# Kernel tuning notes

Measured on AMD Instinct MI355X. Metric: run time of the kernel, lower is better.

## Reference

```python
import jax, jax.numpy as jnp
import numpy as np

N, DEG, F_IN, F_OUT, H = 8192, 16, 1024, 128, 8


def setup_inputs() -> dict:
    key = jax.random.key(0)
    ks = jax.random.split(key, 6)
    features = jax.random.normal(ks[0], (N, F_IN), dtype=jnp.float32)
    adj = jax.random.randint(ks[1], (N, DEG), 0, N)  # fixed-degree adjacency
    W = jax.random.normal(ks[2], (H, F_IN, F_OUT), dtype=jnp.float32) / np.sqrt(F_IN)
    bW = jax.random.normal(ks[3], (H, F_OUT), dtype=jnp.float32) * 0.01
    a = jax.random.normal(ks[4], (H, 2 * F_OUT), dtype=jnp.float32) / np.sqrt(2.0 * F_OUT)
    ba = jax.random.normal(ks[5], (H,), dtype=jnp.float32) * 0.01
    return {"features": features, "adj": adj, "W": W, "bW": bW, "a": a, "ba": ba}


def reference(features, adj, W, bW, a, ba):
    n = features.shape[0]
    # neighbors with self appended last (matches adjlist[node] + [node])
    nbr = jnp.concatenate([adj, jnp.arange(n)[:, None]], axis=1)  # [N, DEG+1]
    # per-head linear transform: h[k] = features @ W_k + b_k
    h = jnp.einsum('nf,hfo->hno', features, W) + bW[:, None, :]  # [H, N, F_OUT]
    # attention score a_k([h_dst, h_src]) + bias decomposed into dst/src parts
    a_dst, a_src = a[:, :F_OUT], a[:, F_OUT:]
    s_dst = jnp.einsum('hno,ho->hn', h, a_dst)  # [H, N]
    s_src = jnp.einsum('hno,ho->hn', h, a_src)  # [H, N]
    scores = s_dst[:, :, None] + s_src[:, nbr] + ba[:, None, None]  # [H, N, DEG+1]
    scores = jax.nn.leaky_relu(scores, 0.2)
    alpha = jax.nn.softmax(scores, axis=-1)  # softmax over neighbors (incl. self)
    h_src = h[:, nbr]  # [H, N, DEG+1, F_OUT]
    out = jnp.einsum('hnd,hndf->hnf', alpha, h_src)  # [H, N, F_OUT]
    # concat heads along feature dim -> [N, H*F_OUT]
    return out.transpose(1, 0, 2).reshape(n, H * F_OUT)
```

## Files before the change

### kernel.cpp

```cpp
#include <hip/hip_runtime.h>
#include <hip/hip_bf16.h>

#define N_NODES 8192
#define DEG     16
#define F_IN    1024
#define F_OUT   128
#define NH      8

typedef __bf16 bf16x8 __attribute__((ext_vector_type(8)));
typedef float  f32x4  __attribute__((ext_vector_type(4)));

__device__ __forceinline__ float bf2f(unsigned short u) {
    union { unsigned int i; float f; } v;
    v.i = ((unsigned int)u) << 16;
    return v.f;
}
__device__ __forceinline__ unsigned short f2bf(float f) {
    union { float f; unsigned int u; } v; v.f = f;
    unsigned int u = v.u + 0x7FFFu + ((v.u >> 16) & 1u);
    return (unsigned short)(u >> 16);
}
__device__ __forceinline__ int detect_bf16(const unsigned int* __restrict__ w) {
    int hits = 0;
#pragma unroll
    for (int i = 0; i < 64; ++i) {
        unsigned int x = w[i * 131 + 17];
        int e = (x >> 7) & 0xFF;
        hits += (e >= 100 && e <= 140) ? 1 : 0;
    }
    return hits > 32;
}
__device__ __forceinline__ float rd_scalar(const void* p, int idx, int isbf) {
    return isbf ? bf2f(((const unsigned short*)p)[idx]) : ((const float*)p)[idx];
}
__device__ __forceinline__ void gload16(const void* g, void* l) {
    __builtin_amdgcn_global_load_lds(
        (const __attribute__((address_space(1))) void*)g,
        (__attribute__((address_space(3))) void*)l, 16, 0, 0);
}

__global__ __launch_bounds__(256) void prep_inputs(
    const void* __restrict__ feat, const void* __restrict__ W,
    unsigned short* __restrict__ featb, unsigned short* __restrict__ Wt)
{
    const int isbf = detect_bf16((const unsigned int*)feat);
    if (blockIdx.x < 4096) {
        size_t i8 = ((size_t)blockIdx.x * 256 + threadIdx.x) * 8;
        if (isbf) {
            *(uint4*)(featb + i8) = ((const uint4*)feat)[i8 / 8];
        } else {
            const float* s = (const float*)feat + i8;
            float4 u0 = *(const float4*)s;
            float4 u1 = *(const float4*)(s + 4);
            unsigned short t[8] = { f2bf(u0.x), f2bf(u0.y), f2bf(u0.z), f2bf(u0.w),
                                    f2bf(u1.x), f2bf(u1.y), f2bf(u1.z), f2bf(u1.w) };
            *(uint4*)(featb + i8) = *(const uint4*)t;
        }
    } else {
        __shared__ float tile[64][65];
        const int bx = blockIdx.x - 4096;
        const int h  = bx >> 5;
        const int kt = (bx >> 1) & 15;
        const int ot = bx & 1;
        const int t  = threadIdx.x;
#pragma unroll
        for (int i = 0; i < 16; ++i) {
            int id = i * 256 + t, r = id >> 6, c = id & 63;
            tile[r][c] = rd_scalar(W, ((h * 1024 + kt * 64 + r) * 128) + ot * 64 + c, isbf);
        }
        __syncthreads();
#pragma unroll
        for (int i = 0; i < 16; ++i) {
            int id = i * 256 + t, oc = id >> 6, kc = id & 63;
            Wt[(size_t)(h * 128 + ot * 64 + oc) * 1024 + kt * 64 + kc] = f2bf(tile[kc][oc]);
        }
    }
}

__global__ __launch_bounds__(512, 4) void gat_gemm6(
    const unsigned short* __restrict__ featb,
    const unsigned short* __restrict__ Wt,
    const void* __restrict__ raw_feat,
    const void* __restrict__ bW, const void* __restrict__ a,
    const void* __restrict__ ba,
    __hip_bfloat16* __restrict__ hbuf,
    float* __restrict__ sdst, float* __restrict__ ssrc)
{
    const int rawbf = detect_bf16((const unsigned int*)raw_feat);

    const int h   = blockIdx.y;
    const int bxp = ((blockIdx.x & 7) << 3) | (blockIdx.x >> 3);
    const int n0  = bxp * 128;
    const int tid = threadIdx.x;

    __shared__ __align__(16) unsigned short As[2][128 * 64];
    __shared__ __align__(16) unsigned short Bs[2][128 * 64];

    const int lane = tid & 63;
    const int wave = tid >> 6;
    const int wr   = wave >> 1;
    const int wc   = wave & 1;
    const int quad = lane >> 4;
    const int l16  = lane & 15;
    const int sw   = l16 & 7;
    const int srow   = lane >> 3;
    const int schunk = lane & 7;

    f32x4 acc[2][4];
#pragma unroll
    for (int i = 0; i < 2; ++i)
#pragma unroll
        for (int j = 0; j < 4; ++j) acc[i][j] = (f32x4)0.f;

    const unsigned short* wbase = Wt + (size_t)h * F_OUT * F_IN;

    for (int k0 = 0; k0 < F_IN; k0 += 128) {
#pragma unroll
        for (int p = 0; p < 2; ++p) {
            const int kk0 = k0 + p * 64;
#pragma unroll
            for (int t = 0; t < 2; ++t) {
                const int r0  = t * 64 + wave * 8;
                const int row = r0 + srow;
                const int gc  = schunk ^ (row & 7);
                gload16(&featb[(size_t)(n0 + row) * F_IN + kk0 + gc * 8],
                        &As[p][r0 * 64]);
                gload16(&wbase[(size_t)row * F_IN + kk0 + gc * 8],
                        &Bs[p][r0 * 64]);
            }
        }
        __syncthreads();

#pragma unroll
        for (int p = 0; p < 2; ++p) {
#pragma unroll
            for (int ks = 0; ks < 2; ++ks) {
                const int kc = ks * 4 + quad;
                const int cs = (kc ^ sw) * 8;
                bf16x8 af[2], bfr[4];
#pragma unroll
                for (int rt = 0; rt < 2; ++rt)
                    af[rt] = *(const bf16x8*)&As[p][(wr * 32 + rt * 16 + l16) * 64 + cs];
#pragma unroll
                for (int ct = 0; ct < 4; ++ct)
                    bfr[ct] = *(const bf16x8*)&Bs[p][(wc * 64 + ct * 16 + l16) * 64 + cs];
#pragma unroll
                for (int rt = 0; rt < 2; ++rt)
#pragma unroll
                    for (int ct = 0; ct < 4; ++ct)
                        acc[rt][ct] = __builtin_amdgcn_mfma_f32_16x16x32_bf16(
                            af[rt], bfr[ct], acc[rt][ct], 0, 0, 0);
            }
        }
        __syncthreads();
    }

#pragma unroll
    for (int ct = 0; ct < 4; ++ct) {
        const int col = wc * 64 + ct * 16 + l16;
        const float bwv = rd_scalar(bW, h * F_OUT + col, rawbf);
#pragma unroll
        for (int rt = 0; rt < 2; ++rt) {
            const int nrow = n0 + wr * 32 + rt * 16 + quad * 4;
            __hip_bfloat16* dst = hbuf + ((size_t)h * N_NODES + nrow) * F_OUT + col;
#pragma unroll
            for (int r = 0; r < 4; ++r)
                dst[(size_t)r * F_OUT] = __float2bfloat16(acc[rt][ct][r] + bwv);
        }
    }

    float adst[4], asrc[4];
#pragma unroll
    for (int ct = 0; ct < 4; ++ct) {
        const int col = wc * 64 + ct * 16 + l16;
        adst[ct] = rd_scalar(a, h * 256 + col, rawbf);
        asrc[ct] = rd_scalar(a, h * 256 + 128 + col, rawbf);
    }
    float pd[2][4] = {}, ps[2][4] = {};
#pragma unroll
    for (int rt = 0; rt < 2; ++rt)
#pragma unroll
        for (int ct = 0; ct < 4; ++ct)
#pragma unroll
            for (int r = 0; r < 4; ++r) {
                pd[rt][r] += acc[rt][ct][r] * adst[ct];
                ps[rt][r] += acc[rt][ct][r] * asrc[ct];
            }
#pragma unroll
    for (int off = 1; off < 16; off <<= 1)
#pragma unroll
        for (int rt = 0; rt < 2; ++rt)
#pragma unroll
            for (int r = 0; r < 4; ++r) {
                pd[rt][r] += __shfl_xor(pd[rt][r], off, 64);
                ps[rt][r] += __shfl_xor(ps[rt][r], off, 64);
            }

    float* sred = (float*)&As[0][0];
    if (l16 == 0) {
#pragma unroll
        for (int rt = 0; rt < 2; ++rt)
#pragma unroll
            for (int r = 0; r < 4; ++r) {
                const int row32 = rt * 16 + quad * 4 + r;
                sred[((wr * 2 + wc) * 2 + 0) * 32 + row32] = pd[rt][r];
                sred[((wr * 2 + wc) * 2 + 1) * 32 + row32] = ps[rt][r];
            }
    }
    __syncthreads();
    if (wc == 0 && lane < 32) {
        const float bav = rd_scalar(ba, h, rawbf);
        const float vd = sred[((wr * 2 + 0) * 2 + 0) * 32 + lane]
                       + sred[((wr * 2 + 1) * 2 + 0) * 32 + lane] + bav;
        const float vs = sred[((wr * 2 + 0) * 2 + 1) * 32 + lane]
                       + sred[((wr * 2 + 1) * 2 + 1) * 32 + lane];
        const int nrow = n0 + wr * 32 + lane;
        sdst[h * N_NODES + nrow] = vd;
        ssrc[h * N_NODES + nrow] = vs;
    }
}

__global__ __launch_bounds__(256) void gat_aggr4(
    const unsigned short* __restrict__ hbuf,
    const int* __restrict__ adj,
    const float* __restrict__ sdst, const float* __restrict__ ssrc,
    const void* __restrict__ raw_feat, void* __restrict__ out)
{
    const int isbf = detect_bf16((const unsigned int*)raw_feat);
    const int h    = blockIdx.x;
    const int wave = threadIdx.x >> 6;
    const int lane = threadIdx.x & 63;
    const int half = lane >> 5;
    const int l32  = lane & 31;
    const int n    = blockIdx.y * 8 + wave * 2 + half;

    int nbr = n;
    if (l32 < DEG) nbr = adj[n * DEG + l32];

    float s = -1e30f;
    if (l32 < 17) {
        float sv = sdst[h * N_NODES + n] + ssrc[h * N_NODES + nbr];
        s = sv > 0.f ? sv : 0.2f * sv;
    }
    float m = s;
#pragma unroll
    for (int off = 1; off < 32; off <<= 1)
        m = fmaxf(m, __shfl_xor(m, off, 64));
    float ev = (l32 < 17) ? __expf(s - m) : 0.f;
    float sum = ev;
#pragma unroll
    for (int off = 1; off < 32; off <<= 1)
        sum += __shfl_xor(sum, off, 64);
    ev *= (1.f / sum);

    const unsigned short* hb = hbuf + (size_t)h * N_NODES * F_OUT;
    const int fc    = l32 * 4;
    const int sbase = half << 5;
    float a0 = 0.f, a1 = 0.f, a2 = 0.f, a3 = 0.f;
#pragma unroll
    for (int d = 0; d < 17; ++d) {
        const int   nb = __shfl(nbr, sbase + d, 64);
        const float av = __shfl(ev,  sbase + d, 64);
        uint2 pk = *(const uint2*)&hb[(size_t)nb * F_OUT + fc];
        a0 += av * bf2f((unsigned short)(pk.x & 0xffffu));
        a1 += av * bf2f((unsigned short)(pk.x >> 16));
        a2 += av * bf2f((unsigned short)(pk.y & 0xffffu));
        a3 += av * bf2f((unsigned short)(pk.y >> 16));
    }

    const size_t oidx = (size_t)n * (NH * F_OUT) + h * F_OUT + fc;
    if (isbf) {
        uint2 res;
        res.x = (unsigned int)f2bf(a0) | ((unsigned int)f2bf(a1) << 16);
        res.y = (unsigned int)f2bf(a2) | ((unsigned int)f2bf(a3) << 16);
        *(uint2*)&((unsigned short*)out)[oidx] = res;
    } else {
        float4 res = { a0, a1, a2, a3 };
        *(float4*)&((float*)out)[oidx] = res;
    }
}

__global__ __launch_bounds__(256) void gat_gemm_fb(
    const void* __restrict__ feat, const void* __restrict__ W,
    const void* __restrict__ bW, __hip_bfloat16* __restrict__ hbuf)
{
    const int isbf = detect_bf16((const unsigned int*)feat);
    const int h = blockIdx.y, n0 = blockIdx.x * 128, tid = threadIdx.x;
    __shared__ __align__(16) unsigned short As[128][72];
    __shared__ __align__(16) unsigned short Bs[128][72];
    const int lane = tid & 63, wave = tid >> 6, quad = lane >> 4, l16 = lane & 15;
    f32x4 acc[2][8];
#pragma unroll
    for (int i = 0; i < 2; ++i)
#pragma unroll
        for (int j = 0; j < 8; ++j) acc[i][j] = (f32x4)0.f;
    for (int k0 = 0; k0 < F_IN; k0 += 64) {
        if (isbf) {
            const unsigned short* fbase = (const unsigned short*)feat + (size_t)n0 * F_IN;
            const unsigned short* wsrc  = (const unsigned short*)W +
                                          (size_t)h * F_IN * F_OUT + (size_t)k0 * F_OUT;
#pragma unroll
            for (int t = 0; t < 4; ++t) {
                int c = t * 256 + tid, row = c >> 3, kc = c & 7;
                *(uint4*)&As[row][kc * 8] = *(const uint4*)&fbase[row * F_IN + k0 + kc * 8];
            }
#pragma unroll
            for (int t = 0; t < 2; ++t) {
                int c = t * 256 + tid, kr2 = c >> 4, mm = c & 15, oc = mm * 8;
                uint4 w0 = *(const uint4*)&wsrc[(2 * kr2) * F_OUT + oc];
                uint4 w1 = *(const uint4*)&wsrc[(2 * kr2 + 1) * F_OUT + oc];
                const unsigned short* p0 = (const unsigned short*)&w0;
                const unsigned short* p1 = (const unsigned short*)&w1;
#pragma unroll
                for (int j = 0; j < 8; ++j) {
                    int i = (j + mm) & 7;
                    *(unsigned int*)&Bs[oc + i][2 * kr2] =
                        (unsigned int)p0[i] | ((unsigned int)p1[i] << 16);
                }
            }
        } else {
            const float* fbase = (const float*)feat + (size_t)n0 * F_IN;
            const float* wsrc  = (const float*)W +
                                 (size_t)h * F_IN * F_OUT + (size_t)k0 * F_OUT;
#pragma unroll
            for (int t = 0; t < 4; ++t) {
                int c = t * 256 + tid, row = c >> 3, kc = c & 7;
                const float* src = &fbase[row * F_IN + k0 + kc * 8];
                float4 u0 = *(const float4*)src, u1 = *(const float4*)(src + 4);
                unsigned short sh[8] = { f2bf(u0.x), f2bf(u0.y), f2bf(u0.z), f2bf(u0.w),
                                         f2bf(u1.x), f2bf(u1.y), f2bf(u1.z), f2bf(u1.w) };
                *(uint4*)&As[row][kc * 8] = *(const uint4*)sh;
            }
#pragma unroll
            for (int t = 0; t < 2; ++t) {
                int c = t * 256 + tid, kr2 = c >> 4, mm = c & 15, oc = mm * 8;
                const float* r0 = &wsrc[(2 * kr2) * F_OUT + oc];
                const float* r1 = &wsrc[(2 * kr2 + 1) * F_OUT + oc];
                float4 e0 = *(const float4*)r0, e1 = *(const float4*)(r0 + 4);
                float4 o0 = *(const float4*)r1, o1 = *(const float4*)(r1 + 4);
                unsigned short p0[8] = { f2bf(e0.x), f2bf(e0.y), f2bf(e0.z), f2bf(e0.w),
                                         f2bf(e1.x), f2bf(e1.y), f2bf(e1.z), f2bf(e1.w) };
                unsigned short p1[8] = { f2bf(o0.x), f2bf(o0.y), f2bf(o0.z), f2bf(o0.w),
                                         f2bf(o1.x), f2bf(o1.y), f2bf(o1.z), f2bf(o1.w) };
#pragma unroll
                for (int j = 0; j < 8; ++j) {
                    int i = (j + mm) & 7;
                    *(unsigned int*)&Bs[oc + i][2 * kr2] =
                        (unsigned int)p0[i] | ((unsigned int)p1[i] << 16);
                }
            }
        }
        __syncthreads();
#pragma unroll
        for (int ks = 0; ks < 2; ++ks) {
            const int kk = ks * 32 + quad * 8;
            bf16x8 af[2], bfr[8];
#pragma unroll
            for (int rt = 0; rt < 2; ++rt)
                af[rt] = *(const bf16x8*)&As[wave * 32 + rt * 16 + l16][kk];
#pragma unroll
            for (int ct = 0; ct < 8; ++ct)
                bfr[ct] = *(const bf16x8*)&Bs[ct * 16 + l16][kk];
#pragma unroll
            for (int rt = 0; rt < 2; ++rt)
#pragma unroll
                for (int ct = 0; ct < 8; ++ct)
                    acc[rt][ct] = __builtin_amdgcn_mfma_f32_16x16x32_bf16(
                        af[rt], bfr[ct], acc[rt][ct], 0, 0, 0);
        }
        __syncthreads();
    }
#pragma unroll
    for (int ct = 0; ct < 8; ++ct) {
        const int col = ct * 16 + l16;
        const float bwv = rd_scalar(bW, h * F_OUT + col, isbf);
#pragma unroll
        for (int rt = 0; rt < 2; ++rt) {
            const int nrow = n0 + wave * 32 + rt * 16 + quad * 4;
            __hip_bfloat16* dst = hbuf + ((size_t)h * N_NODES + nrow) * F_OUT + col;
#pragma unroll
            for (int r = 0; r < 4; ++r)
                dst[(size_t)r * F_OUT] = __float2bfloat16(acc[rt][ct][r] + bwv);
        }
    }
}

__global__ __launch_bounds__(256) void gat_aggr_fb(
    const __hip_bfloat16* __restrict__ hbuf, const int* __restrict__ adj,
    const void* __restrict__ a, const void* __restrict__ ba,
    void* __restrict__ out, const void* __restrict__ feat)
{
    const int isbf = detect_bf16((const unsigned int*)feat);
    const int n = blockIdx.x, wave = threadIdx.x >> 6, lane = threadIdx.x & 63;
    const int hh = blockIdx.y * 4 + wave;
    int nbr_reg = n;
    if (lane < DEG) nbr_reg = adj[n * DEG + lane];
    const int f0 = lane * 2;
    const float adst0 = rd_scalar(a, hh * 256 + f0, isbf);
    const float adst1 = rd_scalar(a, hh * 256 + f0 + 1, isbf);
    const float asrc0 = rd_scalar(a, hh * 256 + 128 + f0, isbf);
    const float asrc1 = rd_scalar(a, hh * 256 + 128 + f0 + 1, isbf);
    const float bav   = rd_scalar(ba, hh, isbf);
    const __hip_bfloat16* hb = hbuf + (size_t)hh * N_NODES * F_OUT;
    float v0[17], v1[17], red[18];
#pragma unroll
    for (int d = 0; d < 17; ++d) {
        int nb = __shfl(nbr_reg, d, 64);
        unsigned int pk = *(const unsigned int*)&hb[(size_t)nb * F_OUT + f0];
        v0[d] = bf2f((unsigned short)(pk & 0xffffu));
        v1[d] = bf2f((unsigned short)(pk >> 16));
        red[d] = v0[d] * asrc0 + v1[d] * asrc1;
    }
    red[17] = v0[16] * adst0 + v1[16] * adst1;
#pragma unroll
    for (int off = 1; off < 64; off <<= 1)
#pragma unroll
        for (int r = 0; r < 18; ++r) red[r] += __shfl_xor(red[r], off, 64);
    const float sd = red[17] + bav;
    float sc[17], mx = -1e30f;
#pragma unroll
    for (int d = 0; d < 17; ++d) {
        float s = sd + red[d];
        s = s > 0.f ? s : 0.2f * s;
        sc[d] = s; mx = fmaxf(mx, s);
    }
    float ssum = 0.f;
#pragma unroll
    for (int d = 0; d < 17; ++d) { sc[d] = __expf(sc[d] - mx); ssum += sc[d]; }
    const float inv = 1.f / ssum;
    float o0 = 0.f, o1 = 0.f;
#pragma unroll
    for (int d = 0; d < 17; ++d) { o0 += sc[d] * v0[d]; o1 += sc[d] * v1[d]; }
    o0 *= inv; o1 *= inv;
    const size_t oidx = (size_t)n * (NH * F_OUT) + hh * F_OUT + f0;
    if (isbf) {
        *(unsigned int*)&((unsigned short*)out)[oidx] =
            (unsigned int)f2bf(o0) | ((unsigned int)f2bf(o1) << 16);
    } else {
        float2 res; res.x = o0; res.y = o1;
        *(float2*)&((float*)out)[oidx] = res;
    }
}

extern "C" void kernel_launch(void* const* d_in, const int* in_sizes, int n_in,
                              void* d_out, int out_size, void* d_ws, size_t ws_size,
                              hipStream_t stream)
{
    const void* feat = d_in[0];
    const int*  adj  = (const int*)d_in[1];
    const void* W    = d_in[2];
    const void* bW   = d_in[3];
    const void* a    = d_in[4];
    const void* ba   = d_in[5];

    char* ws = (char*)d_ws;
    __hip_bfloat16* hbuf = (__hip_bfloat16*)ws;
    const size_t HB = (size_t)NH * N_NODES * F_OUT * 2;
    const size_t SC = (size_t)NH * N_NODES * 4;
    float* sdst = (float*)(ws + HB);
    float* ssrc = (float*)(ws + HB + SC);
    unsigned short* featb = (unsigned short*)(ws + HB + 2 * SC);
    unsigned short* Wt    = featb + (size_t)N_NODES * F_IN;
    const size_t needA = HB + 2 * SC +
        ((size_t)N_NODES * F_IN + (size_t)NH * F_IN * F_OUT) * 2;

    if (ws_size >= needA) {
        prep_inputs<<<4352, 256, 0, stream>>>(feat, W, featb, Wt);
        gat_gemm6<<<dim3(64, 8), 512, 0, stream>>>(featb, Wt, feat, bW, a, ba,
                                                   hbuf, sdst, ssrc);
        gat_aggr4<<<dim3(8, 1024), 256, 0, stream>>>((const unsigned short*)hbuf,
                                                     adj, sdst, ssrc, feat, d_out);
    } else {
        gat_gemm_fb<<<dim3(64, 8), 256, 0, stream>>>(feat, W, bW, hbuf);
        gat_aggr_fb<<<dim3(8192, 2), 256, 0, stream>>>(hbuf, adj, a, ba, d_out, feat);
    }
}
```

Measured before the change: 148.1 us.

## Load GEMM B-operand fragments directly from global into registers with double buffering

The W (B operand) tile is no longer staged through shared memory. Each wave now reads its bf16x8 fragments straight from global or L2 into registers and prefetches the next k-step while the current MFMAs run. This halves LDS usage, which may allow more blocks per CU, and removes the LDS reads for B. The cost is uncoalesced 16-byte global loads across rows and duplicate W reads, since every wave row-group fetches the same fragments.

```diff
diff --git a/kernel.cpp b/kernel.cpp
--- a/kernel.cpp
+++ b/kernel.cpp
@@ -77,7 +77,7 @@
     }
 }
 
-__global__ __launch_bounds__(512, 4) void gat_gemm6(
+__global__ __launch_bounds__(512, 4) void gat_gemm7(
     const unsigned short* __restrict__ featb,
     const unsigned short* __restrict__ Wt,
     const void* __restrict__ raw_feat,
@@ -94,7 +94,6 @@
     const int tid = threadIdx.x;
 
     __shared__ __align__(16) unsigned short As[2][128 * 64];
-    __shared__ __align__(16) unsigned short Bs[2][128 * 64];
 
     const int lane = tid & 63;
     const int wave = tid >> 6;
@@ -114,6 +113,18 @@
 
     const unsigned short* wbase = Wt + (size_t)h * F_OUT * F_IN;
 
+    bf16x8 bb[2][4];
+    auto loadB = [&](int k0, int step, int buf) {
+        const int p  = step >> 1;
+        const int ks = step & 1;
+        const int kk = k0 + p * 64 + (ks * 4 + quad) * 8;
+#pragma unroll
+        for (int ct = 0; ct < 4; ++ct) {
+            const int col = wc * 64 + ct * 16 + l16;
+            bb[buf][ct] = *(const bf16x8*)&wbase[(size_t)col * F_IN + kk];
+        }
+    };
+
     for (int k0 = 0; k0 < F_IN; k0 += 128) {
 #pragma unroll
         for (int p = 0; p < 2; ++p) {
@@ -125,32 +136,29 @@
                 const int gc  = schunk ^ (row & 7);
                 gload16(&featb[(size_t)(n0 + row) * F_IN + kk0 + gc * 8],
                         &As[p][r0 * 64]);
-                gload16(&wbase[(size_t)row * F_IN + kk0 + gc * 8],
-                        &Bs[p][r0 * 64]);
-            }
-        }
+            }
+        }
+        loadB(k0, 0, 0);
         __syncthreads();
 
 #pragma unroll
-        for (int p = 0; p < 2; ++p) {
-#pragma unroll
-            for (int ks = 0; ks < 2; ++ks) {
-                const int kc = ks * 4 + quad;
-                const int cs = (kc ^ sw) * 8;
-                bf16x8 af[2], bfr[4];
-#pragma unroll
-                for (int rt = 0; rt < 2; ++rt)
-                    af[rt] = *(const bf16x8*)&As[p][(wr * 32 + rt * 16 + l16) * 64 + cs];
+        for (int step = 0; step < 4; ++step) {
+            const int p  = step >> 1;
+            const int ks = step & 1;
+            if (step < 3) loadB(k0, step + 1, (step + 1) & 1);
+
+            const int kc = ks * 4 + quad;
+            const int cs = (kc ^ sw) * 8;
+            bf16x8 af[2];
+#pragma unroll
+            for (int rt = 0; rt < 2; ++rt)
+                af[rt] = *(const bf16x8*)&As[p][(wr * 32 + rt * 16 + l16) * 64 + cs];
+#pragma unroll
+            for (int rt = 0; rt < 2; ++rt)
 #pragma unroll
                 for (int ct = 0; ct < 4; ++ct)
-                    bfr[ct] = *(const bf16x8*)&Bs[p][(wc * 64 + ct * 16 + l16) * 64 + cs];
-#pragma unroll
-                for (int rt = 0; rt < 2; ++rt)
-#pragma unroll
-                    for (int ct = 0; ct < 4; ++ct)
-                        acc[rt][ct] = __builtin_amdgcn_mfma_f32_16x16x32_bf16(
-                            af[rt], bfr[ct], acc[rt][ct], 0, 0, 0);
-            }
+                    acc[rt][ct] = __builtin_amdgcn_mfma_f32_16x16x32_bf16(
+                        af[rt], bb[step & 1][ct], acc[rt][ct], 0, 0, 0);
         }
         __syncthreads();
     }
@@ -466,7 +474,7 @@
 
     if (ws_size >= needA) {
         prep_inputs<<<4352, 256, 0, stream>>>(feat, W, featb, Wt);
-        gat_gemm6<<<dim3(64, 8), 512, 0, stream>>>(featb, Wt, feat, bW, a, ba,
+        gat_gemm7<<<dim3(64, 8), 512, 0, stream>>>(featb, Wt, feat, bW, a, ba,
                                                    hbuf, sdst, ssrc);
         gat_aggr4<<<dim3(8, 1024), 256, 0, stream>>>((const unsigned short*)hbuf,
                                                      adj, sdst, ssrc, feat, d_out);
```

After: 193.4 us. +30.6%, slower.
